# Kernel optimization log

Measured on AMD Instinct MI355X. Metric: run time of the kernel, lower is better.

The kernel has to match this reference:

```python
import jax, jax.numpy as jnp
import numpy as np

N_QUBITS = 10
N_GEN = 4
Q_DEPTH = 6
BATCH = 1024


def _cz_chain_diag(n):
    # Diagonal of the CZ chain CZ(0,1) CZ(1,2) ... CZ(n-2,n-1):
    # phase (-1)^(# adjacent 1-1 pairs) per computational basis state.
    idx = np.arange(2 ** n)
    bits = (idx[:, None] >> np.arange(n - 1, -1, -1)) & 1  # wire 0 = most significant (PennyLane)
    pairs = (bits[:, :-1] & bits[:, 1:]).sum(axis=1)
    return ((-1.0) ** pairs).astype(np.float32).reshape((2,) * n)

_CZ = jnp.asarray(_cz_chain_diag(N_QUBITS))


def _ry(t):
    c = jnp.cos(0.5 * t)
    s = jnp.sin(0.5 * t)
    return jnp.stack([jnp.stack([c, -s]), jnp.stack([s, c])]).astype(jnp.complex64)


def _rx(t):
    c = jnp.cos(0.5 * t).astype(jnp.complex64)
    js = (1j * jnp.sin(0.5 * t)).astype(jnp.complex64)
    return jnp.stack([jnp.stack([c, -js]), jnp.stack([-js, c])])


def _apply_1q(state, gate, wire):
    # state: (2,)*n complex statevector; apply 2x2 gate on `wire`.
    state = jnp.moveaxis(state, wire, -1)
    state = jnp.einsum('...j,ij->...i', state, gate)
    return jnp.moveaxis(state, -1, wire)


def _circuit(noise_s, weights, cz):
    # noise_s: (n_qubits,), weights: (q_depth, n_qubits)
    n = noise_s.shape[0]
    state = jnp.zeros((2,) * n, jnp.complex64).at[(0,) * n].set(1.0)
    for q in range(n):
        state = _apply_1q(state, _ry(noise_s[q]), q)
        state = _apply_1q(state, _rx(noise_s[q]), q)

    def layer(st, w):
        for q in range(n):
            st = _apply_1q(st, _ry(w[q]), q)
        return st * cz, None

    state, _ = jax.lax.scan(layer, state, weights)
    # <X_q> = Re <psi| X_q |psi>; X_q flips the q-th wire.
    return jnp.stack([jnp.real(jnp.vdot(state, jnp.flip(state, axis=q))) for q in range(n)])


def setup_inputs() -> dict:
    key = jax.random.key(0)
    k1, k2 = jax.random.split(key)
    noise = jax.random.normal(k1, (BATCH, N_QUBITS), dtype=jnp.float32)
    q_params = jax.random.uniform(k2, (N_GEN, Q_DEPTH, N_QUBITS), dtype=jnp.float32)  # q_delta=1.0 * rand
    return {"noise": noise, "q_params": q_params}


def reference(noise, q_params):
    per_sample = lambda ns, w: _circuit(ns, w, _CZ)
    per_gen = jax.vmap(lambda w: jax.vmap(lambda ns: per_sample(ns, w))(noise))(q_params)  # (G, B, n)
    out = jnp.transpose(per_gen, (1, 0, 2)).reshape(noise.shape[0], N_GEN * N_QUBITS)
    return out.astype(jnp.float32)
```

## Files before the change

### kernel.cpp

```cpp
#include <hip/hip_runtime.h>

#define NQ 10
#define NG 4
#define QD 6
#define NBATCH 1024
#define WPB 4


typedef unsigned u2v __attribute__((ext_vector_type(2)));

template<int CTRL, int RM, int BM, bool BC>
__device__ __forceinline__ float dppmov(float x) {
    return __int_as_float(__builtin_amdgcn_update_dpp(
        0, __float_as_int(x), CTRL, RM, BM, BC));
}
template<int CTRL>
__device__ __forceinline__ float dpp1(float x) { return dppmov<CTRL,0xF,0xF,true>(x); }

struct FX1 { static __device__ __forceinline__ float f(float x){ return dpp1<0xB1>(x); } };
struct FX2 { static __device__ __forceinline__ float f(float x){ return dpp1<0x4E>(x); } };
struct FX4 { static __device__ __forceinline__ float f(float x){ return dpp1<0x1B>(dpp1<0x141>(x)); } };
struct FX8 { static __device__ __forceinline__ float f(float x){ return dpp1<0x128>(x); } };
struct FX16 {
    static __device__ __forceinline__ float f(float x){
        return __int_as_float(__builtin_amdgcn_ds_swizzle(__float_as_int(x), 0x401F));
    }
};
struct FX32 {
    static __device__ __forceinline__ float f(float x){ return __shfl_xor(x, 32, 64); }
};

__device__ __forceinline__ float rlane(float v, int idx) {
    return __int_as_float(__builtin_amdgcn_readlane(__float_as_int(v), idx));
}

#if __has_builtin(__builtin_amdgcn_permlane32_swap) && __has_builtin(__builtin_amdgcn_permlane16_swap)
#define HAVE_SWAP 1
__device__ __forceinline__ void plswap32(float &a, float &b) {
    u2v r = __builtin_amdgcn_permlane32_swap(__float_as_uint(a), __float_as_uint(b), false, false);
    a = __uint_as_float(r.x); b = __uint_as_float(r.y);
}
__device__ __forceinline__ void plswap16(float &a, float &b) {
    u2v r = __builtin_amdgcn_permlane16_swap(__float_as_uint(a), __float_as_uint(b), false, false);
    a = __uint_as_float(r.x); b = __uint_as_float(r.y);
}
__device__ __forceinline__ void tr_b5b3(float (&s)[16]) {
#pragma unroll
    for (int j = 0; j < 8; ++j) plswap32(s[j], s[j + 8]);
}
__device__ __forceinline__ void tr_b4b2(float (&s)[16]) {
#pragma unroll
    for (int jj = 0; jj < 8; ++jj) {
        const int j = (jj & 3) | ((jj >> 2) << 3);
        plswap16(s[j], s[j + 4]);
    }
}
#else
#define HAVE_SWAP 0
#endif

__device__ __forceinline__ float wave_reduce(float x) {
    x += dppmov<0x111,0xF,0xF,true >(x);
    x += dppmov<0x112,0xF,0xF,true >(x);
    x += dppmov<0x114,0xF,0xF,true >(x);
    x += dppmov<0x118,0xF,0xF,true >(x);
    x += dppmov<0x142,0xA,0xF,false>(x);
    x += dppmov<0x143,0xC,0xF,false>(x);
    return __int_as_float(__builtin_amdgcn_readlane(__float_as_int(x), 63));
}

__device__ __forceinline__ float wave_product(float x) {
    x *= dpp1<0xB1>(x);
    x *= dpp1<0x4E>(x);
    x *= dpp1<0x1B>(dpp1<0x141>(x));
    x *= dpp1<0x128>(x);
    x *= FX16::f(x);
    x *= FX32::f(x);
    return x;
}

template<int M>
__device__ __forceinline__ void intra_rot_t(float (&s)[16], float t) {
#pragma unroll
    for (int j = 0; j < 16; ++j)
        if ((j & M) == 0) {
            const int k = j | M;
            float v0 = s[j], v1 = s[k];
            s[j] = fmaf(-t, v1, v0);
            s[k] = fmaf( t, v0, v1);
        }
}

template<class PF, int LM>
__device__ __forceinline__ void cross_rot_t(float (&sr)[16], float (&si)[16],
                                            float t, int lane) {
    const float sv = (lane & LM) ? t : -t;
#pragma unroll
    for (int j = 0; j < 16; ++j) {
        sr[j] = fmaf(PF::f(sr[j]), sv, sr[j]);
        si[j] = fmaf(PF::f(si[j]), sv, si[j]);
    }
}

template<class PF>
__device__ __forceinline__ float cross_exp(const float (&sr)[16], const float (&si)[16]) {
    float a = 0.f;
#pragma unroll
    for (int j = 0; j < 16; ++j) {
        a = fmaf(PF::f(sr[j]), sr[j], a);
        a = fmaf(PF::f(si[j]), si[j], a);
    }
    return a;
}

template<int M>
__device__ __forceinline__ float intra_exp(const float (&sr)[16], const float (&si)[16]) {
    float a = 0.f;
#pragma unroll
    for (int j = 0; j < 16; ++j)
        a += sr[j] * sr[j ^ M] + si[j] * si[j ^ M];
    return a;
}

__global__ __launch_bounds__(256, 2) void qsim_kernel(
    const float* __restrict__ noise,
    const float* __restrict__ qp,
    float* __restrict__ out)
{
    const int wave = threadIdx.x >> 6;
    const int lane = threadIdx.x & 63;
    const int g    = blockIdx.x & 3;
    const int b    = (blockIdx.x >> 2) * WPB + wave;

    float wt, scale2;
    {
        const int widx = (lane < QD * NQ) ? lane : 0;
        float sv, cv;
        __sincosf(0.5f * qp[g * (QD * NQ) + widx], &sv, &cv);
        wt = sv / cv;
        float cvc = (lane < QD * NQ) ? cv : 1.0f;
        float p = wave_product(cvc);
        scale2 = p * p;
    }

    float sr[16], si[16];
    {
        float nc[NQ], ns[NQ];
#pragma unroll
        for (int q = 0; q < NQ; ++q)
            __sincosf(0.5f * noise[b * NQ + q], &ns[q], &nc[q]);

        auto facr = [&](int q, int bit) { return bit ? nc[q]*ns[q] : nc[q]*nc[q]; };
        auto faci = [&](int q, int bit) { return bit ? -nc[q]*ns[q] : -ns[q]*ns[q]; };

        float hr = 1.f, hi = 0.f;
#pragma unroll
        for (int p = 4; p <= 9; ++p) {
            const int q = NQ - 1 - p, bit = (lane >> (p - 4)) & 1;
            float fr = facr(q, bit), fi = faci(q, bit);
            float tr = hr * fr - hi * fi;
            float ti = hr * fi + hi * fr;
            hr = tr; hi = ti;
        }
        float t01r[4], t01i[4], t23r[4], t23i[4];
#pragma unroll
        for (int a = 0; a < 4; ++a) {
            float f9r = facr(9, a & 1), f9i = faci(9, a & 1);
            float f8r = facr(8, (a >> 1) & 1), f8i = faci(8, (a >> 1) & 1);
            t01r[a] = f9r * f8r - f9i * f8i;
            t01i[a] = f9r * f8i + f9i * f8r;
            float f7r = facr(7, a & 1), f7i = faci(7, a & 1);
            float f6r = facr(6, (a >> 1) & 1), f6i = faci(6, (a >> 1) & 1);
            t23r[a] = f7r * f6r - f7i * f6i;
            t23i[a] = f7r * f6i + f7i * f6r;
        }
        float prer[4], prei[4];
#pragma unroll
        for (int a = 0; a < 4; ++a) {
            prer[a] = hr * t01r[a] - hi * t01i[a];
            prei[a] = hr * t01i[a] + hi * t01r[a];
        }
#pragma unroll
        for (int j = 0; j < 16; ++j) {
            sr[j] = prer[j & 3] * t23r[j >> 2] - prei[j & 3] * t23i[j >> 2];
            si[j] = prer[j & 3] * t23i[j >> 2] + prei[j & 3] * t23r[j >> 2];
        }
    }

    unsigned mE, mEn, mO, mOn;
    {
        unsigned par_l = (unsigned)(__popc(lane & (lane >> 1)) & 1) << 31;
        mE  = par_l;
        mEn = mE ^ 0x80000000u;
        mO  = mE ^ ((unsigned)(lane & 1) << 31);
        mOn = mO ^ 0x80000000u;
    }

#pragma unroll 1
    for (int l = 0; l < QD; ++l) {
        const int base = l * NQ;
        float t[NQ];
#pragma unroll
        for (int q = 0; q < NQ; ++q) t[q] = rlane(wt, base + q);

        intra_rot_t<1>(sr, t[9]); intra_rot_t<1>(si, t[9]);
        intra_rot_t<2>(sr, t[8]); intra_rot_t<2>(si, t[8]);
        intra_rot_t<4>(sr, t[7]); intra_rot_t<4>(si, t[7]);
        intra_rot_t<8>(sr, t[6]); intra_rot_t<8>(si, t[6]);
        cross_rot_t<FX1, 1>(sr, si, t[5], lane);
        cross_rot_t<FX2, 2>(sr, si, t[4], lane);
        cross_rot_t<FX4, 4>(sr, si, t[3], lane);
        cross_rot_t<FX8, 8>(sr, si, t[2], lane);
#if HAVE_SWAP
        tr_b5b3(sr); tr_b5b3(si);
        tr_b4b2(sr); tr_b4b2(si);
        intra_rot_t<8>(sr, t[0]); intra_rot_t<8>(si, t[0]);
        intra_rot_t<4>(sr, t[1]); intra_rot_t<4>(si, t[1]);
        tr_b4b2(sr); tr_b4b2(si);
        tr_b5b3(sr); tr_b5b3(si);
#else
        cross_rot_t<FX32,32>(sr, si, t[0], lane);
        cross_rot_t<FX16,16>(sr, si, t[1], lane);
#endif
#pragma unroll
        for (int j = 0; j < 16; ++j) {
            const bool jpar = (__popc(j & (j >> 1)) & 1) != 0;
            const unsigned m = (j & 8) ? (jpar ? mOn : mO) : (jpar ? mEn : mE);
            sr[j] = __uint_as_float(__float_as_uint(sr[j]) ^ m);
            si[j] = __uint_as_float(__float_as_uint(si[j]) ^ m);
        }
    }

    float outval = 0.f;
    {
        float e9 = wave_reduce(intra_exp<1>(sr, si));
        float e8 = wave_reduce(intra_exp<2>(sr, si));
        float e7 = wave_reduce(intra_exp<4>(sr, si));
        float e6 = wave_reduce(intra_exp<8>(sr, si));
        float e5 = wave_reduce(cross_exp<FX1>(sr, si));
        float e4 = wave_reduce(cross_exp<FX2>(sr, si));
        float e3 = wave_reduce(cross_exp<FX4>(sr, si));
        float e2 = wave_reduce(cross_exp<FX8>(sr, si));
        float e0, e1;
#if HAVE_SWAP
        tr_b5b3(sr); tr_b5b3(si);
        tr_b4b2(sr); tr_b4b2(si);
        e0 = wave_reduce(intra_exp<8>(sr, si));
        e1 = wave_reduce(intra_exp<4>(sr, si));
#else
        e0 = wave_reduce(cross_exp<FX32>(sr, si));
        e1 = wave_reduce(cross_exp<FX16>(sr, si));
#endif
        outval = (lane == 0) ? e0 : outval;
        outval = (lane == 1) ? e1 : outval;
        outval = (lane == 2) ? e2 : outval;
        outval = (lane == 3) ? e3 : outval;
        outval = (lane == 4) ? e4 : outval;
        outval = (lane == 5) ? e5 : outval;
        outval = (lane == 6) ? e6 : outval;
        outval = (lane == 7) ? e7 : outval;
        outval = (lane == 8) ? e8 : outval;
        outval = (lane == 9) ? e9 : outval;
    }

    if (lane < NQ)
        out[b * (NG * NQ) + g * NQ + lane] = outval * scale2;
}

extern "C" void kernel_launch(void* const* d_in, const int* in_sizes, int n_in,
                              void* d_out, int out_size, void* d_ws, size_t ws_size,
                              hipStream_t stream) {
    const float* noise = (const float*)d_in[0];
    const float* qp    = (const float*)d_in[1];
    float* out = (float*)d_out;

    const int nblocks = (NBATCH * NG) / WPB;
    qsim_kernel<<<nblocks, 64 * WPB, 0, stream>>>(noise, qp, out);
}
```

Measured before the change: 87.61 us.

## Alternate qubit-to-lane layouts across layers to halve permlane transposes

The state vector is no longer transposed back to its original layout after each layer. Layers are processed in pairs: the second layer runs in the swapped layout, and a second CZ sign mask (czB) is derived for that layout, so each layer needs one transpose set instead of two. The FX4 and FX8 lane exchanges also change from DPP sequences to ds_swizzle. This removes permlane swap traffic, but ds_swizzle goes through the LDS crossbar and may be slower than DPP, and the new sign-mask derivation must be exactly right.

```diff
diff --git a/kernel.cpp b/kernel.cpp
--- a/kernel.cpp
+++ b/kernel.cpp
@@ -17,18 +17,17 @@
 template<int CTRL>
 __device__ __forceinline__ float dpp1(float x) { return dppmov<CTRL,0xF,0xF,true>(x); }
 
+template<int PAT>
+__device__ __forceinline__ float swz(float x) {
+    return __int_as_float(__builtin_amdgcn_ds_swizzle(__float_as_int(x), PAT));
+}
+
 struct FX1 { static __device__ __forceinline__ float f(float x){ return dpp1<0xB1>(x); } };
 struct FX2 { static __device__ __forceinline__ float f(float x){ return dpp1<0x4E>(x); } };
-struct FX4 { static __device__ __forceinline__ float f(float x){ return dpp1<0x1B>(dpp1<0x141>(x)); } };
-struct FX8 { static __device__ __forceinline__ float f(float x){ return dpp1<0x128>(x); } };
-struct FX16 {
-    static __device__ __forceinline__ float f(float x){
-        return __int_as_float(__builtin_amdgcn_ds_swizzle(__float_as_int(x), 0x401F));
-    }
-};
-struct FX32 {
-    static __device__ __forceinline__ float f(float x){ return __shfl_xor(x, 32, 64); }
-};
+struct FX4 { static __device__ __forceinline__ float f(float x){ return swz<0x101F>(x); } };
+struct FX8 { static __device__ __forceinline__ float f(float x){ return swz<0x201F>(x); } };
+struct FX16{ static __device__ __forceinline__ float f(float x){ return swz<0x401F>(x); } };
+struct FX32{ static __device__ __forceinline__ float f(float x){ return __shfl_xor(x, 32, 64); } };
 
 __device__ __forceinline__ float rlane(float v, int idx) {
     return __int_as_float(__builtin_amdgcn_readlane(__float_as_int(v), idx));
@@ -44,11 +43,9 @@
     u2v r = __builtin_amdgcn_permlane16_swap(__float_as_uint(a), __float_as_uint(b), false, false);
     a = __uint_as_float(r.x); b = __uint_as_float(r.y);
 }
-__device__ __forceinline__ void tr_b5b3(float (&s)[16]) {
+__device__ __forceinline__ void tr_set(float (&s)[16]) {
 #pragma unroll
     for (int j = 0; j < 8; ++j) plswap32(s[j], s[j + 8]);
-}
-__device__ __forceinline__ void tr_b4b2(float (&s)[16]) {
 #pragma unroll
     for (int jj = 0; jj < 8; ++jj) {
         const int j = (jj & 3) | ((jj >> 2) << 3);
@@ -72,38 +69,43 @@
 __device__ __forceinline__ float wave_product(float x) {
     x *= dpp1<0xB1>(x);
     x *= dpp1<0x4E>(x);
-    x *= dpp1<0x1B>(dpp1<0x141>(x));
-    x *= dpp1<0x128>(x);
+    x *= FX4::f(x);
+    x *= FX8::f(x);
     x *= FX16::f(x);
     x *= FX32::f(x);
     return x;
 }
 
 template<int M>
-__device__ __forceinline__ void intra_rot_t(float (&s)[16], float t) {
+__device__ __forceinline__ void intra2(float (&sr)[16], float (&si)[16], float t) {
 #pragma unroll
     for (int j = 0; j < 16; ++j)
         if ((j & M) == 0) {
             const int k = j | M;
-            float v0 = s[j], v1 = s[k];
-            s[j] = fmaf(-t, v1, v0);
-            s[k] = fmaf( t, v0, v1);
+            float r0 = sr[j], r1 = sr[k];
+            sr[j] = fmaf(-t, r1, r0);
+            sr[k] = fmaf( t, r0, r1);
+            float i0 = si[j], i1 = si[k];
+            si[j] = fmaf(-t, i1, i0);
+            si[k] = fmaf( t, i0, i1);
         }
 }
 
 template<class PF, int LM>
-__device__ __forceinline__ void cross_rot_t(float (&sr)[16], float (&si)[16],
-                                            float t, int lane) {
+__device__ __forceinline__ void cross2(float (&sr)[16], float (&si)[16],
+                                       float t, int lane) {
     const float sv = (lane & LM) ? t : -t;
 #pragma unroll
     for (int j = 0; j < 16; ++j) {
-        sr[j] = fmaf(PF::f(sr[j]), sv, sr[j]);
-        si[j] = fmaf(PF::f(si[j]), sv, si[j]);
+        float pr = PF::f(sr[j]);
+        float pi = PF::f(si[j]);
+        sr[j] = fmaf(pr, sv, sr[j]);
+        si[j] = fmaf(pi, sv, si[j]);
     }
 }
 
 template<class PF>
-__device__ __forceinline__ float cross_exp(const float (&sr)[16], const float (&si)[16]) {
+__device__ __forceinline__ float cross_exp2(const float (&sr)[16], const float (&si)[16]) {
     float a = 0.f;
 #pragma unroll
     for (int j = 0; j < 16; ++j) {
@@ -114,7 +116,7 @@
 }
 
 template<int M>
-__device__ __forceinline__ float intra_exp(const float (&sr)[16], const float (&si)[16]) {
+__device__ __forceinline__ float intra_exp2(const float (&sr)[16], const float (&si)[16]) {
     float a = 0.f;
 #pragma unroll
     for (int j = 0; j < 16; ++j)
@@ -187,69 +189,115 @@
         }
     }
 
-    unsigned mE, mEn, mO, mOn;
-    {
-        unsigned par_l = (unsigned)(__popc(lane & (lane >> 1)) & 1) << 31;
-        mE  = par_l;
-        mEn = mE ^ 0x80000000u;
-        mO  = mE ^ ((unsigned)(lane & 1) << 31);
-        mOn = mO ^ 0x80000000u;
-    }
-
+    unsigned aE, aO;
+    {
+        unsigned parA = (unsigned)(__popc(lane & (lane >> 1)) & 1) << 31;
+        aE = parA;
+        aO = parA ^ ((unsigned)(lane & 1) << 31);
+    }
+    unsigned b00, b10, b01, b11;
+    {
+        const unsigned l0 = lane & 1, l1 = (lane >> 1) & 1, l2 = (lane >> 2) & 1,
+                       l3 = (lane >> 3) & 1, l4 = (lane >> 4) & 1, l5 = (lane >> 5) & 1;
+        unsigned parB = ((l4 & l5) ^ (l5 & l0) ^ (l0 & l1) ^ (l1 & l2) ^ (l2 & l3)) << 31;
+        b00 = parB;
+        b10 = parB ^ (l4 << 31);
+        b01 = parB ^ (l3 << 31);
+        b11 = parB ^ ((l4 ^ l3) << 31);
+    }
+    auto czA = [&](float (&vr)[16], float (&vi)[16]) {
+#pragma unroll
+        for (int j = 0; j < 16; ++j) {
+            const bool jp = (__popc(j & (j >> 1)) & 1) != 0;
+            const unsigned base = (j & 8) ? aO : aE;
+            const unsigned m = jp ? (base ^ 0x80000000u) : base;
+            vr[j] = __uint_as_float(__float_as_uint(vr[j]) ^ m);
+            vi[j] = __uint_as_float(__float_as_uint(vi[j]) ^ m);
+        }
+    };
+    auto czB = [&](float (&vr)[16], float (&vi)[16]) {
+#pragma unroll
+        for (int j = 0; j < 16; ++j) {
+            const int j0 = j & 1, j1 = (j >> 1) & 1, j2 = (j >> 2) & 1, j3 = (j >> 3) & 1;
+            const bool pj = ((j0 & j1) ^ (j2 & j3)) != 0;
+            const unsigned base = j1 ? (j2 ? b11 : b10) : (j2 ? b01 : b00);
+            const unsigned m = pj ? (base ^ 0x80000000u) : base;
+            vr[j] = __uint_as_float(__float_as_uint(vr[j]) ^ m);
+            vi[j] = __uint_as_float(__float_as_uint(vi[j]) ^ m);
+        }
+    };
+
+#if HAVE_SWAP
+#pragma unroll 1
+    for (int d = 0; d < QD / 2; ++d) {
+        float t[2 * NQ];
+#pragma unroll
+        for (int q = 0; q < 2 * NQ; ++q) t[q] = rlane(wt, 2 * d * NQ + q);
+
+        intra2<1>(sr, si, t[9]);
+        intra2<2>(sr, si, t[8]);
+        intra2<4>(sr, si, t[7]);
+        intra2<8>(sr, si, t[6]);
+        cross2<FX1, 1>(sr, si, t[5], lane);
+        cross2<FX2, 2>(sr, si, t[4], lane);
+        cross2<FX4, 4>(sr, si, t[3], lane);
+        cross2<FX8, 8>(sr, si, t[2], lane);
+        tr_set(sr); tr_set(si);
+        intra2<8>(sr, si, t[0]);
+        intra2<4>(sr, si, t[1]);
+        czB(sr, si);
+
+        intra2<1>(sr, si, t[NQ + 9]);
+        intra2<2>(sr, si, t[NQ + 8]);
+        intra2<8>(sr, si, t[NQ + 0]);
+        intra2<4>(sr, si, t[NQ + 1]);
+        cross2<FX1, 1>(sr, si, t[NQ + 5], lane);
+        cross2<FX2, 2>(sr, si, t[NQ + 4], lane);
+        cross2<FX4, 4>(sr, si, t[NQ + 3], lane);
+        cross2<FX8, 8>(sr, si, t[NQ + 2], lane);
+        tr_set(sr); tr_set(si);
+        intra2<4>(sr, si, t[NQ + 7]);
+        intra2<8>(sr, si, t[NQ + 6]);
+        czA(sr, si);
+    }
+#else
 #pragma unroll 1
     for (int l = 0; l < QD; ++l) {
-        const int base = l * NQ;
         float t[NQ];
 #pragma unroll
-        for (int q = 0; q < NQ; ++q) t[q] = rlane(wt, base + q);
-
-        intra_rot_t<1>(sr, t[9]); intra_rot_t<1>(si, t[9]);
-        intra_rot_t<2>(sr, t[8]); intra_rot_t<2>(si, t[8]);
-        intra_rot_t<4>(sr, t[7]); intra_rot_t<4>(si, t[7]);
-        intra_rot_t<8>(sr, t[6]); intra_rot_t<8>(si, t[6]);
-        cross_rot_t<FX1, 1>(sr, si, t[5], lane);
-        cross_rot_t<FX2, 2>(sr, si, t[4], lane);
-        cross_rot_t<FX4, 4>(sr, si, t[3], lane);
-        cross_rot_t<FX8, 8>(sr, si, t[2], lane);
-#if HAVE_SWAP
-        tr_b5b3(sr); tr_b5b3(si);
-        tr_b4b2(sr); tr_b4b2(si);
-        intra_rot_t<8>(sr, t[0]); intra_rot_t<8>(si, t[0]);
-        intra_rot_t<4>(sr, t[1]); intra_rot_t<4>(si, t[1]);
-        tr_b4b2(sr); tr_b4b2(si);
-        tr_b5b3(sr); tr_b5b3(si);
-#else
-        cross_rot_t<FX32,32>(sr, si, t[0], lane);
-        cross_rot_t<FX16,16>(sr, si, t[1], lane);
+        for (int q = 0; q < NQ; ++q) t[q] = rlane(wt, l * NQ + q);
+        intra2<1>(sr, si, t[9]);
+        intra2<2>(sr, si, t[8]);
+        intra2<4>(sr, si, t[7]);
+        intra2<8>(sr, si, t[6]);
+        cross2<FX1, 1>(sr, si, t[5], lane);
+        cross2<FX2, 2>(sr, si, t[4], lane);
+        cross2<FX4, 4>(sr, si, t[3], lane);
+        cross2<FX8, 8>(sr, si, t[2], lane);
+        cross2<FX32,32>(sr, si, t[0], lane);
+        cross2<FX16,16>(sr, si, t[1], lane);
+        czA(sr, si);
+    }
 #endif
-#pragma unroll
-        for (int j = 0; j < 16; ++j) {
-            const bool jpar = (__popc(j & (j >> 1)) & 1) != 0;
-            const unsigned m = (j & 8) ? (jpar ? mOn : mO) : (jpar ? mEn : mE);
-            sr[j] = __uint_as_float(__float_as_uint(sr[j]) ^ m);
-            si[j] = __uint_as_float(__float_as_uint(si[j]) ^ m);
-        }
-    }
 
     float outval = 0.f;
     {
-        float e9 = wave_reduce(intra_exp<1>(sr, si));
-        float e8 = wave_reduce(intra_exp<2>(sr, si));
-        float e7 = wave_reduce(intra_exp<4>(sr, si));
-        float e6 = wave_reduce(intra_exp<8>(sr, si));
-        float e5 = wave_reduce(cross_exp<FX1>(sr, si));
-        float e4 = wave_reduce(cross_exp<FX2>(sr, si));
-        float e3 = wave_reduce(cross_exp<FX4>(sr, si));
-        float e2 = wave_reduce(cross_exp<FX8>(sr, si));
+        float e9 = wave_reduce(intra_exp2<1>(sr, si));
+        float e8 = wave_reduce(intra_exp2<2>(sr, si));
+        float e7 = wave_reduce(intra_exp2<4>(sr, si));
+        float e6 = wave_reduce(intra_exp2<8>(sr, si));
+        float e5 = wave_reduce(cross_exp2<FX1>(sr, si));
+        float e4 = wave_reduce(cross_exp2<FX2>(sr, si));
+        float e3 = wave_reduce(cross_exp2<FX4>(sr, si));
+        float e2 = wave_reduce(cross_exp2<FX8>(sr, si));
         float e0, e1;
 #if HAVE_SWAP
-        tr_b5b3(sr); tr_b5b3(si);
-        tr_b4b2(sr); tr_b4b2(si);
-        e0 = wave_reduce(intra_exp<8>(sr, si));
-        e1 = wave_reduce(intra_exp<4>(sr, si));
+        tr_set(sr); tr_set(si);
+        e0 = wave_reduce(intra_exp2<8>(sr, si));
+        e1 = wave_reduce(intra_exp2<4>(sr, si));
 #else
-        e0 = wave_reduce(cross_exp<FX32>(sr, si));
-        e1 = wave_reduce(cross_exp<FX16>(sr, si));
+        e0 = wave_reduce(cross_exp2<FX32>(sr, si));
+        e1 = wave_reduce(cross_exp2<FX16>(sr, si));
 #endif
         outval = (lane == 0) ? e0 : outval;
         outval = (lane == 1) ? e1 : outval;
```

Result: faster. 85.09 us (-2.9%).
